# Kernel optimization log

Measured on AMD Instinct MI355X. Metric: run time of the kernel, lower is better.

Reference implementation:

```python
import jax, jax.numpy as jnp
import numpy as np

B, F, H, T = 32, 128, 256, 2048


def setup_inputs() -> dict:
    key = jax.random.key(0)
    ks = jax.random.split(key, 20)
    s = 0.05
    x = jax.random.normal(ks[0], (B, 1, T, F), dtype=jnp.float32)
    mask = (jax.random.uniform(ks[1], (B, 1, T, F)) < 0.5).astype(jnp.float32)
    delta = jax.random.uniform(ks[2], (B, 1, T, F), dtype=jnp.float32)  # time since last obs
    inp = jnp.concatenate([x, mask, delta], axis=1)  # [B, 3, T, F]
    p = lambda k, shape: jax.random.normal(k, shape, dtype=jnp.float32) * s
    return {
        "input": inp,
        "x_mean": p(ks[3], (F,)),
        # layer 0: input decay (diagonal), hidden decay, gates
        "w_dx": p(ks[4], (F,)), "b_dx": p(ks[5], (F,)),
        "W_dh0": p(ks[6], (F, H)), "b_dh0": p(ks[7], (H,)),
        "W0": p(ks[8], (F, 3 * H)), "U0": p(ks[9], (H, 3 * H)),
        "V0": p(ks[10], (F, 3 * H)), "b0": p(ks[11], (3 * H,)),
        # layer 1: hidden decay from delta, gates (input = prev layer hidden)
        "W_dh1": p(ks[12], (F, H)), "b_dh1": p(ks[13], (H,)),
        "W1": p(ks[14], (H, 3 * H)), "U1": p(ks[15], (H, 3 * H)),
        "V1": p(ks[16], (F, 3 * H)), "b1": p(ks[17], (3 * H,)),
    }


def _grud_cell(x_in, m, delta, h, W_dh, b_dh, W, U, V, b):
    # hidden-state decay from delta-time
    gamma_h = jnp.exp(-jax.nn.relu(delta @ W_dh + b_dh))  # [B,H]
    h = gamma_h * h
    pre = x_in @ W + m @ V + b                             # [B,3H]
    hU = h @ U[:, : 2 * H]                                 # r,z recurrent terms
    r = jax.nn.sigmoid(pre[:, :H] + hU[:, :H])
    z = jax.nn.sigmoid(pre[:, H : 2 * H] + hU[:, H : 2 * H])
    h_tilde = jnp.tanh(pre[:, 2 * H :] + (r * h) @ U[:, 2 * H :])
    return (1.0 - z) * h + z * h_tilde


def reference(input, x_mean, w_dx, b_dx, W_dh0, b_dh0, W0, U0, V0, b0,
              W_dh1, b_dh1, W1, U1, V1, b1):
    xs = jnp.moveaxis(input, 2, 0)  # [T, B, 3, F]
    x_last0 = jnp.broadcast_to(x_mean, (B, F))
    h0 = jnp.zeros((B, H), dtype=input.dtype)
    h1 = jnp.zeros((B, H), dtype=input.dtype)

    def step(carry, inp_t):
        x_last, h0, h1 = carry
        x, m, delta = inp_t[:, 0], inp_t[:, 1], inp_t[:, 2]  # [B,F] each
        # input decay toward empirical mean (GRU-D imputation)
        gamma_x = jnp.exp(-jax.nn.relu(delta * w_dx + b_dx))
        x_hat = m * x + (1.0 - m) * (gamma_x * x_last + (1.0 - gamma_x) * x_mean)
        h0n = _grud_cell(x_hat, m, delta, h0, W_dh0, b_dh0, W0, U0, V0, b0)
        h1n = _grud_cell(h0n, m, delta, h1, W_dh1, b_dh1, W1, U1, V1, b1)
        x_last_new = jnp.where(m > 0, x, x_last)  # update AFTER the cells, as in torch
        return (x_last_new, h0n, h1n), h1n

    _, ys = jax.lax.scan(step, (x_last0, h0, h1), xs)
    return ys  # [T, B, H]
```

## Files before the change

kernel.cpp:

```cpp
#include <hip/hip_runtime.h>

typedef _Float16 f16;
typedef _Float16 f16x2 __attribute__((ext_vector_type(2)));
typedef unsigned int u32;

#define CB 32
#define CF 128
#define CH 256
#define CT 2048
#define TCC 128
#define SEG 16
#define SLEN 128
#define SHBYTES 16896

static __device__ __forceinline__ f16x2 bc(u32 u){ return __builtin_bit_cast(f16x2, u); }
static __device__ __forceinline__ u32 packh2(float lo, float hi){ f16x2 v; v.x=(f16)lo; v.y=(f16)hi; return __builtin_bit_cast(u32, v); }

static __device__ __forceinline__ float dot2f(f16x2 a, f16x2 b, float c){
#if defined(__has_builtin)
#if __has_builtin(__builtin_amdgcn_fdot2)
  return __builtin_amdgcn_fdot2(a, b, c, false);
#else
  return c + (float)a.x*(float)b.x + (float)a.y*(float)b.y;
#endif
#else
  return c + (float)a.x*(float)b.x + (float)a.y*(float)b.y;
#endif
}
static __device__ __forceinline__ float dot4q(float acc, uint4 w, uint4 h){
  acc = dot2f(bc(w.x), bc(h.x), acc);
  acc = dot2f(bc(w.y), bc(h.y), acc);
  acc = dot2f(bc(w.z), bc(h.z), acc);
  acc = dot2f(bc(w.w), bc(h.w), acc);
  return acc;
}

#define PIN4(V) asm volatile("" : "+v"((V).x), "+v"((V).y), "+v"((V).z), "+v"((V).w))

#define RBAR() do { \
  asm volatile("s_waitcnt lgkmcnt(0)" ::: "memory"); \
  __builtin_amdgcn_s_barrier(); \
  asm volatile("" ::: "memory"); \
} while (0)

__global__ void init_hst(float* hst){
  int i = blockIdx.x*256 + threadIdx.x;
  if (i < 2*CB*CH) hst[i] = 0.f;
}

static __device__ __forceinline__ float wc0src(int k, int n, const float* W0, const float* V0, const float* Wdh0){
  if (k < 128) return (n < 768) ? W0[k*768 + n] : 0.f;
  if (k < 256) return (n < 768) ? V0[(k-128)*768 + n] : 0.f;
  return (n >= 768) ? Wdh0[(k-256)*256 + (n-768)] : 0.f;
}
static __device__ __forceinline__ float wc1src(int k, int n, const float* W1, const float* V1, const float* Wdh1){
  if (k < 256) return (n < 768) ? W1[k*768 + n] : 0.f;
  if (k < 384) return (n < 768) ? V1[(k-256)*768 + n] : 0.f;
  return (n >= 768) ? Wdh1[(k-384)*256 + (n-768)] : 0.f;
}
static __device__ __forceinline__ u32 wrz_pair(int flat, int jj, int L, const float* U){
  int p = L >> 2, q = L & 3;
  int cc = flat >> 3, j = flat & 7;
  int col = 4*p + cc;
  int pr = 32*q + 4*j + jj;
  return packh2(U[(2*pr)*768 + col], U[(2*pr+1)*768 + col]);
}
static __device__ __forceinline__ u32 wcc_pair(int flat, int jj, int L, const float* U){
  int p = L >> 2, q = L & 3;
  int cc2 = flat >> 3, j = flat & 7;
  int col = 512 + 2*p + cc2;
  int pr = 32*q + 4*j + jj;
  return packh2(U[(2*pr)*768 + col], U[(2*pr+1)*768 + col]);
}

__global__ __launch_bounds__(256) void pack_w(
    const float* __restrict__ W0, const float* __restrict__ V0, const float* __restrict__ Wdh0,
    const float* __restrict__ W1, const float* __restrict__ V1, const float* __restrict__ Wdh1,
    const float* __restrict__ U0, const float* __restrict__ U1,
    const float* __restrict__ b0, const float* __restrict__ bdh0,
    const float* __restrict__ b1, const float* __restrict__ bdh1,
    u32* __restrict__ WC0p, u32* __restrict__ WC1p,
    u32* __restrict__ WRZa, u32* __restrict__ WRZb,
    u32* __restrict__ WCCa, u32* __restrict__ WCCb,
    float* __restrict__ bias0, float* __restrict__ bias1){
  int idx = blockIdx.x*256 + threadIdx.x;
  if (idx < 196608){
    int k2 = idx >> 10, n = idx & 1023;
    WC0p[idx] = packh2(wc0src(2*k2, n, W0,V0,Wdh0), wc0src(2*k2+1, n, W0,V0,Wdh0));
  } else if (idx < 458752){
    int j = idx - 196608; int k2 = j >> 10, n = j & 1023;
    WC1p[j] = packh2(wc1src(2*k2, n, W1,V1,Wdh1), wc1src(2*k2+1, n, W1,V1,Wdh1));
  } else if (idx < 524288){
    int j = idx - 458752; int flat = j >> 11, L = (j >> 2) & 511, jj = j & 3;
    WRZa[j] = wrz_pair(flat, jj, L, U0);
  } else if (idx < 589824){
    int j = idx - 524288; int flat = j >> 11, L = (j >> 2) & 511, jj = j & 3;
    WRZb[j] = wrz_pair(flat, jj, L, U1);
  } else if (idx < 622592){
    int j = idx - 589824; int flat = j >> 11, L = (j >> 2) & 511, jj = j & 3;
    WCCa[j] = wcc_pair(flat, jj, L, U0);
  } else if (idx < 655360){
    int j = idx - 622592; int flat = j >> 11, L = (j >> 2) & 511, jj = j & 3;
    WCCb[j] = wcc_pair(flat, jj, L, U1);
  } else if (idx < 657408){
    int i = idx - 655360;
    if (i < 1024) bias0[i] = (i < 768) ? b0[i] : bdh0[i - 768];
    else { int j = i - 1024; bias1[j] = (j < 768) ? b1[j] : bdh1[j - 768]; }
  }
}

__global__ __launch_bounds__(256) void k1a(const float* __restrict__ in,
    float* __restrict__ segval, int* __restrict__ seghas){
  int tid = blockIdx.x*256 + threadIdx.x;
  int s = tid >> 12, chain = tid & 4095;
  int b = chain >> 7, f = chain & 127;
  const float* px = in + ((size_t)b*3 + 0)*CT*CF + f;
  const float* pm = in + ((size_t)b*3 + 1)*CT*CF + f;
  float last = 0.f; int has = 0;
  #pragma unroll 4
  for (int u = 0; u < SLEN; ++u){
    int t = s*SLEN + u;
    float m = pm[(size_t)t*CF], x = px[(size_t)t*CF];
    if (m > 0.f){ last = x; has = 1; }
  }
  segval[s*4096 + chain] = last;
  seghas[s*4096 + chain] = has;
}
__global__ __launch_bounds__(256) void k1b(const float* __restrict__ x_mean,
    const float* __restrict__ segval, const int* __restrict__ seghas, float* __restrict__ seed){
  int chain = blockIdx.x*256 + threadIdx.x;
  int f = chain & 127;
  float cur = x_mean[f];
  #pragma unroll
  for (int s = 0; s < SEG; ++s){
    seed[s*4096 + chain] = cur;
    if (seghas[s*4096 + chain]) cur = segval[s*4096 + chain];
  }
}
__global__ __launch_bounds__(256) void k1c(const float* __restrict__ in, const float* __restrict__ x_mean,
    const float* __restrict__ w_dx, const float* __restrict__ b_dx,
    const float* __restrict__ seed, f16* __restrict__ A){
  int tid = blockIdx.x*256 + threadIdx.x;
  int s = tid >> 12, chain = tid & 4095;
  int b = chain >> 7, f = chain & 127;
  const float wd = w_dx[f], bd = b_dx[f], xm = x_mean[f];
  const float* px = in + ((size_t)b*3 + 0)*CT*CF + f;
  const float* pm = in + ((size_t)b*3 + 1)*CT*CF + f;
  const float* pd = in + ((size_t)b*3 + 2)*CT*CF + f;
  float xl = seed[s*4096 + chain];
  #pragma unroll 4
  for (int u = 0; u < SLEN; ++u){
    int t = s*SLEN + u;
    float x = px[(size_t)t*CF], m = pm[(size_t)t*CF], d = pd[(size_t)t*CF];
    float gx = __expf(-fmaxf(d*wd + bd, 0.f));
    float xh = m*x + (1.f-m)*(gx*xl + (1.f-gx)*xm);
    f16* wq = A + ((size_t)t*CB + b)*384 + f;
    wq[0] = (f16)xh; wq[128] = (f16)m; wq[256] = (f16)d;
    xl = (m > 0.f) ? x : xl;
  }
}

static __device__ void gemm_tile(
    const u32* __restrict__ Aa, int lda, const u32* __restrict__ Ab, int ldb, int kasplit,
    int ktiles, const u32* __restrict__ Wp, const float* __restrict__ bias, float* __restrict__ Out,
    int row0, int n0, int tid, char* sm){
  u32 (*AsT)[68] = (u32 (*)[68])sm;
  u32 (*Bs)[64]  = (u32 (*)[64])(sm + 4352);
  const int tx = tid & 15, ty = tid >> 4;
  const int am = tid >> 2, akq = (tid & 3) * 4;
  const int bk = tid >> 4, bnq = (tid & 15) * 4;
  float acc[4][4] = {};
  for (int kt = 0; kt < ktiles; ++kt){
    int k2g = kt*16 + akq;
    uint4 ga;
    if (k2g < kasplit) ga = *(const uint4*)&Aa[(size_t)(row0 + am)*lda + k2g];
    else               ga = *(const uint4*)&Ab[(size_t)(row0 + am)*ldb + (k2g - kasplit)];
    uint4 gb = *(const uint4*)&Wp[(size_t)(kt*16 + bk)*1024 + n0 + bnq];
    __syncthreads();
    AsT[akq+0][am] = ga.x; AsT[akq+1][am] = ga.y; AsT[akq+2][am] = ga.z; AsT[akq+3][am] = ga.w;
    *(uint4*)&Bs[bk][bnq] = gb;
    __syncthreads();
    #pragma unroll
    for (int kk = 0; kk < 16; ++kk){
      uint4 bq = *(const uint4*)&Bs[kk][tx*4];
      uint4 aq = *(const uint4*)&AsT[kk][ty*4];
      f16x2 bv0 = bc(bq.x), bv1 = bc(bq.y), bv2 = bc(bq.z), bv3 = bc(bq.w);
      f16x2 av0 = bc(aq.x), av1 = bc(aq.y), av2 = bc(aq.z), av3 = bc(aq.w);
      acc[0][0] = dot2f(av0, bv0, acc[0][0]); acc[0][1] = dot2f(av0, bv1, acc[0][1]);
      acc[0][2] = dot2f(av0, bv2, acc[0][2]); acc[0][3] = dot2f(av0, bv3, acc[0][3]);
      acc[1][0] = dot2f(av1, bv0, acc[1][0]); acc[1][1] = dot2f(av1, bv1, acc[1][1]);
      acc[1][2] = dot2f(av1, bv2, acc[1][2]); acc[1][3] = dot2f(av1, bv3, acc[1][3]);
      acc[2][0] = dot2f(av2, bv0, acc[2][0]); acc[2][1] = dot2f(av2, bv1, acc[2][1]);
      acc[2][2] = dot2f(av2, bv2, acc[2][2]); acc[2][3] = dot2f(av2, bv3, acc[2][3]);
      acc[3][0] = dot2f(av3, bv0, acc[3][0]); acc[3][1] = dot2f(av3, bv1, acc[3][1]);
      acc[3][2] = dot2f(av3, bv2, acc[3][2]); acc[3][3] = dot2f(av3, bv3, acc[3][3]);
    }
  }
  const bool isg = (n0 >= 768);
  #pragma unroll
  for (int i = 0; i < 4; ++i){
    int r = row0 + ty*4 + i;
    int n = n0 + tx*4;
    float4 v;
    float* vv = (float*)&v;
    #pragma unroll
    for (int j = 0; j < 4; ++j){
      float x = acc[i][j] + bias[n + j];
      if (isg) x = __expf(-fmaxf(x, 0.f));
      vv[j] = x;
    }
    *(float4*)&Out[(size_t)r*1024 + n] = v;
  }
}

__global__ __launch_bounds__(512, 2) void mega(
    const float* __restrict__ O0r, const float* __restrict__ O1r,
    const u32* __restrict__ WRZa, const u32* __restrict__ WRZb,
    const u32* __restrict__ WCCa, const u32* __restrict__ WCCb,
    float* __restrict__ hst, f16* __restrict__ h0cw, float* __restrict__ out,
    int t0_l1, int n0, int n1, int g0n, int g1n,
    const u32* __restrict__ g0a, float* __restrict__ g0out,
    const u32* __restrict__ g1a, const u32* __restrict__ g1b, float* __restrict__ g1out,
    const u32* __restrict__ WC0p, const u32* __restrict__ WC1p,
    const float* __restrict__ bias0, const float* __restrict__ bias1){
  extern __shared__ __align__(16) char smraw[];
  const int L = threadIdx.x;
  if (blockIdx.x >= 64){
    int gb = blockIdx.x - 64;
    int st = L >> 8, t2 = L & 255;
    char* smst = smraw + st*8448;
    if (gb < g0n){
      int tile = gb*2 + st;
      gemm_tile(g0a, 192, g0a, 192, 192, 12, WC0p, bias0, g0out, (tile>>4)*64, (tile&15)*64, t2, smst);
    } else {
      int tile = (gb - g0n)*2 + st;
      gemm_tile(g1a, 128, g1b, 192, 128, 16, WC1p, bias1, g1out, (tile>>4)*64, (tile&15)*64, t2, smst);
    }
    return;
  }
  const int role = blockIdx.x >> 5;
  const int b = blockIdx.x & 31;
  const int steps = role ? n1 : n0;
  if (steps == 0) return;
  const float* O = role ? O1r : O0r;
  const u32* WRZ = role ? WRZb : WRZa;
  const u32* WCC = role ? WCCb : WCCa;
  float* hcarry = hst + role*CB*CH;

  f16*  hdh_  = (f16*)(smraw);
  f16*  rh_   = (f16*)(smraw + 640);
  float* hdf  = (float*)(smraw + 1280);
  float* zz   = (float*)(smraw + 2304);

  uint4 wrz[32];
  #pragma unroll
  for (int i = 0; i < 32; ++i) wrz[i] = *(const uint4*)&WRZ[((size_t)i*512 + L)*4];
  uint4 wcc[16];
  #pragma unroll
  for (int i = 0; i < 16; ++i) wcc[i] = *(const uint4*)&WCC[((size_t)i*512 + L)*4];
  #pragma unroll
  for (int i = 0; i < 32; ++i) PIN4(wrz[i]);
  #pragma unroll
  for (int i = 0; i < 16; ++i) PIN4(wcc[i]);

  const int p = L >> 2, q = L & 3;
  size_t row = (size_t)b*1024;
  if (L < 256){
    float hd = O[row + 768 + L] * hcarry[b*256 + L];
    hdf[L] = hd; hdh_[(L>>6)*80 + (L&63)] = (f16)hd;
  }
  float prz = O[row + L];
  const int e2 = 2*p + (q & 1);
  float pc = (q < 2) ? O[row + 512 + e2] : 0.f;
  const char* hqb = (const char*)hdh_ + q*160;
  const char* rqb = (const char*)rh_ + q*160;
  __syncthreads();

  for (int lt = 0; lt < steps; ++lt){
    size_t nrow = row + (size_t)CB*1024;
    float nprz = 0.f, npc = 0.f, ngex = 0.f;
    if (lt + 1 < steps){
      nprz = O[nrow + L];
      if (q < 2){ npc = O[nrow + 512 + e2]; ngex = O[nrow + 768 + e2]; }
    }
    float hdL = (L < 256) ? hdf[L] : 0.f;
    float hd2 = hdf[e2];
    float a0=0.f, a1=0.f, a2=0.f, a3=0.f;
    #pragma unroll
    for (int j = 0; j < 8; ++j){
      uint4 h = ((const uint4*)hqb)[j];
      a0 = dot4q(a0, wrz[j],      h);
      a1 = dot4q(a1, wrz[8 + j],  h);
      a2 = dot4q(a2, wrz[16 + j], h);
      a3 = dot4q(a3, wrz[24 + j], h);
    }
    a0 += __shfl_xor(a0, 1); a1 += __shfl_xor(a1, 1); a2 += __shfl_xor(a2, 1); a3 += __shfl_xor(a3, 1);
    a0 += __shfl_xor(a0, 2); a1 += __shfl_xor(a1, 2); a2 += __shfl_xor(a2, 2); a3 += __shfl_xor(a3, 2);
    float sum1 = (q == 0) ? a0 : (q == 1) ? a1 : (q == 2) ? a2 : a3;
    float s1 = 1.f/(1.f + __expf(-(sum1 + prz)));
    if (L < 256) rh_[(L>>6)*80 + (L&63)] = (f16)(s1 * hdL);
    else zz[L - 256] = s1;
    RBAR();
    float z = zz[e2];
    float b0_=0.f, b1_=0.f;
    #pragma unroll
    for (int j = 0; j < 8; ++j){
      uint4 r = ((const uint4*)rqb)[j];
      b0_ = dot4q(b0_, wcc[j],     r);
      b1_ = dot4q(b1_, wcc[8 + j], r);
    }
    b0_ += __shfl_xor(b0_, 1); b1_ += __shfl_xor(b1_, 1);
    b0_ += __shfl_xor(b0_, 2); b1_ += __shfl_xor(b1_, 2);
    if (q < 2){
      float sumc = (q & 1) ? b1_ : b0_;
      float v = pc + sumc;
      float e = __expf(2.f*v);
      float ct = 1.f - 2.f/(1.f + e);
      float hd = hd2;
      float hn = hd + z*(ct - hd);
      float hdn = ngex*hn;
      hdf[e2] = hdn; hdh_[(e2>>6)*80 + (e2&63)] = (f16)hdn;
      if (role == 0) h0cw[((size_t)lt*CB + b)*256 + e2] = (f16)hn;
      else           out[((size_t)(t0_l1 + lt)*CB + b)*256 + e2] = hn;
      if (lt == steps-1) hcarry[b*256 + e2] = hn;
    }
    prz = nprz; pc = npc;
    row = nrow;
    RBAR();
  }
}

extern "C" void kernel_launch(void* const* d_in, const int* in_sizes, int n_in,
                              void* d_out, int out_size, void* d_ws, size_t ws_size,
                              hipStream_t stream){
  const float* input  = (const float*)d_in[0];
  const float* x_mean = (const float*)d_in[1];
  const float* w_dx   = (const float*)d_in[2];
  const float* b_dx   = (const float*)d_in[3];
  const float* Wdh0   = (const float*)d_in[4];
  const float* bdh0   = (const float*)d_in[5];
  const float* W0     = (const float*)d_in[6];
  const float* U0     = (const float*)d_in[7];
  const float* V0     = (const float*)d_in[8];
  const float* b0     = (const float*)d_in[9];
  const float* Wdh1   = (const float*)d_in[10];
  const float* bdh1   = (const float*)d_in[11];
  const float* W1     = (const float*)d_in[12];
  const float* U1     = (const float*)d_in[13];
  const float* V1     = (const float*)d_in[14];
  const float* b1     = (const float*)d_in[15];
  float* out = (float*)d_out;

  hipFuncSetAttribute((const void*)mega, hipFuncAttributeMaxDynamicSharedMemorySize, SHBYTES);

  char* base = (char*)d_ws;
  size_t off = 0;
  auto take = [&](size_t bytes)->char*{
    char* p = base + off;
    off = (off + bytes + 255) & ~(size_t)255;
    return p;
  };
  f16*  IN0h  = (f16*) take((size_t)CT*CB*384*2);
  u32*  WC0p  = (u32*) take((size_t)192*1024*4);
  u32*  WC1p  = (u32*) take((size_t)256*1024*4);
  u32*  WRZa  = (u32*) take((size_t)32*512*4*4);
  u32*  WRZb  = (u32*) take((size_t)32*512*4*4);
  u32*  WCCa  = (u32*) take((size_t)16*512*4*4);
  u32*  WCCb  = (u32*) take((size_t)16*512*4*4);
  float* bias0= (float*)take(1024*4);
  float* bias1= (float*)take(1024*4);
  float* hst  = (float*)take((size_t)2*CB*CH*4);
  float* segv = (float*)take((size_t)SEG*4096*4);
  int*   segh = (int*)  take((size_t)SEG*4096*4);
  float* seed = (float*)take((size_t)SEG*4096*4);
  float* O0b[2], *O1b[2]; f16* h0b[2];
  O0b[0] = (float*)take((size_t)TCC*CB*1024*4);
  O0b[1] = (float*)take((size_t)TCC*CB*1024*4);
  O1b[0] = (float*)take((size_t)TCC*CB*1024*4);
  O1b[1] = (float*)take((size_t)TCC*CB*1024*4);
  h0b[0] = (f16*)  take((size_t)TCC*CB*CH*2);
  h0b[1] = (f16*)  take((size_t)TCC*CB*CH*2);

  hipLaunchKernelGGL(init_hst, dim3(64), dim3(256), 0, stream, hst);
  hipLaunchKernelGGL(pack_w, dim3((657408 + 255)/256), dim3(256), 0, stream,
      W0, V0, Wdh0, W1, V1, Wdh1, U0, U1, b0, bdh0, b1, bdh1,
      WC0p, WC1p, WRZa, WRZb, WCCa, WCCb, bias0, bias1);
  hipLaunchKernelGGL(k1a, dim3(256), dim3(256), 0, stream, input, segv, segh);
  hipLaunchKernelGGL(k1b, dim3(16), dim3(256), 0, stream, x_mean, segv, segh, seed);
  hipLaunchKernelGGL(k1c, dim3(256), dim3(256), 0, stream, input, x_mean, w_dx, b_dx, seed, IN0h);

  const u32* IN0p = (const u32*)IN0h;
  const int nch = CT / TCC;
  for (int i = -1; i <= nch + 1; ++i){
    int r0 = (i >= 0 && i < nch) ? 1 : 0;
    int r1 = (i >= 2 && i < nch + 2) ? 1 : 0;
    int g0 = (i + 1 >= 0 && i + 1 < nch) ? 1 : 0;
    int g1 = (i - 1 >= 0 && i - 1 < nch) ? 1 : 0;
    int g0n = g0 ? 512 : 0, g1n = g1 ? 512 : 0;
    const float* O0r = O0b[i & 1];
    const float* O1r = O1b[i & 1];
    f16* h0cw = h0b[i & 1];
    const u32* g0a = IN0p + (size_t)(i+1)*TCC*CB*192;
    float* g0out = O0b[(i+1) & 1];
    const u32* g1a = (const u32*)h0b[(i-1) & 1];
    const u32* g1b = IN0p + (size_t)(i-1)*TCC*CB*192 + 64;
    float* g1out = O1b[(i-1) & 1];
    hipLaunchKernelGGL(mega, dim3(64 + g0n + g1n), dim3(512), SHBYTES, stream,
        O0r, O1r, WRZa, WRZb, WCCa, WCCb, hst, h0cw, out,
        (i-2)*TCC, r0 ? TCC : 0, r1 ? TCC : 0, g0n, g1n,
        g0a, g0out, g1a, g1b, g1out,
        WC0p, WC1p, bias0, bias1);
  }
}
```

Baseline: 3.760 ms.

## Batch recurrent GRU steps over 16 rows per block using MFMA

The recurrent part of each GRU-D cell now runs in 4 blocks, each handling 16 batch rows and both gate matmuls with 16x16x32 f16 MFMA instructions, instead of 64 blocks each doing one batch row with fdot2 dot products and cross-lane shuffles. The U weights are repacked into MFMA fragment layout and hidden states are staged in padded LDS tiles. This cuts per-step instruction count and shuffle reductions, but it leaves far fewer blocks on the serial critical path and uses more LDS per block.

```diff
diff --git a/kernel.cpp b/kernel.cpp
--- a/kernel.cpp
+++ b/kernel.cpp
@@ -2,6 +2,8 @@
 
 typedef _Float16 f16;
 typedef _Float16 f16x2 __attribute__((ext_vector_type(2)));
+typedef _Float16 f16x8 __attribute__((ext_vector_type(8)));
+typedef float f32x4 __attribute__((ext_vector_type(4)));
 typedef unsigned int u32;
 
 #define CB 32
@@ -11,9 +13,10 @@
 #define TCC 128
 #define SEG 16
 #define SLEN 128
-#define SHBYTES 16896
+#define SHBYTES 58368
 
 static __device__ __forceinline__ f16x2 bc(u32 u){ return __builtin_bit_cast(f16x2, u); }
+static __device__ __forceinline__ f16x8 bch8(uint4 u){ return __builtin_bit_cast(f16x8, u); }
 static __device__ __forceinline__ u32 packh2(float lo, float hi){ f16x2 v; v.x=(f16)lo; v.y=(f16)hi; return __builtin_bit_cast(u32, v); }
 
 static __device__ __forceinline__ float dot2f(f16x2 a, f16x2 b, float c){
@@ -27,13 +30,6 @@
   return c + (float)a.x*(float)b.x + (float)a.y*(float)b.y;
 #endif
 }
-static __device__ __forceinline__ float dot4q(float acc, uint4 w, uint4 h){
-  acc = dot2f(bc(w.x), bc(h.x), acc);
-  acc = dot2f(bc(w.y), bc(h.y), acc);
-  acc = dot2f(bc(w.z), bc(h.z), acc);
-  acc = dot2f(bc(w.w), bc(h.w), acc);
-  return acc;
-}
 
 #define PIN4(V) asm volatile("" : "+v"((V).x), "+v"((V).y), "+v"((V).z), "+v"((V).w))
 
@@ -58,19 +54,19 @@
   if (k < 384) return (n < 768) ? V1[(k-256)*768 + n] : 0.f;
   return (n >= 768) ? Wdh1[(k-384)*256 + (n-768)] : 0.f;
 }
-static __device__ __forceinline__ u32 wrz_pair(int flat, int jj, int L, const float* U){
-  int p = L >> 2, q = L & 3;
-  int cc = flat >> 3, j = flat & 7;
-  int col = 4*p + cc;
-  int pr = 32*q + 4*j + jj;
-  return packh2(U[(2*pr)*768 + col], U[(2*pr+1)*768 + col]);
-}
-static __device__ __forceinline__ u32 wcc_pair(int flat, int jj, int L, const float* U){
-  int p = L >> 2, q = L & 3;
-  int cc2 = flat >> 3, j = flat & 7;
-  int col = 512 + 2*p + cc2;
-  int pr = 32*q + 4*j + jj;
-  return packh2(U[(2*pr)*768 + col], U[(2*pr+1)*768 + col]);
+static __device__ __forceinline__ u32 wfrz_src(int j, const float* U){
+  int fi = j >> 11, Lt = (j >> 2) & 511, d = j & 3;
+  int wv = Lt >> 6, lg = (Lt >> 4) & 3, li = Lt & 15;
+  int col = 64*wv + 16*(fi >> 3) + li;
+  int k0 = (fi & 7)*32 + lg*8 + 2*d;
+  return packh2(U[k0*768 + col], U[(k0+1)*768 + col]);
+}
+static __device__ __forceinline__ u32 wfc_src(int j, const float* U){
+  int fi = j >> 11, Lt = (j >> 2) & 511, d = j & 3;
+  int wv = Lt >> 6, lg = (Lt >> 4) & 3, li = Lt & 15;
+  int col = 512 + 32*wv + 16*(fi >> 3) + li;
+  int k0 = (fi & 7)*32 + lg*8 + 2*d;
+  return packh2(U[k0*768 + col], U[(k0+1)*768 + col]);
 }
 
 __global__ __launch_bounds__(256) void pack_w(
@@ -80,8 +76,8 @@
     const float* __restrict__ b0, const float* __restrict__ bdh0,
     const float* __restrict__ b1, const float* __restrict__ bdh1,
     u32* __restrict__ WC0p, u32* __restrict__ WC1p,
-    u32* __restrict__ WRZa, u32* __restrict__ WRZb,
-    u32* __restrict__ WCCa, u32* __restrict__ WCCb,
+    u32* __restrict__ WF0rz, u32* __restrict__ WF1rz,
+    u32* __restrict__ WF0c, u32* __restrict__ WF1c,
     float* __restrict__ bias0, float* __restrict__ bias1){
   int idx = blockIdx.x*256 + threadIdx.x;
   if (idx < 196608){
@@ -91,17 +87,13 @@
     int j = idx - 196608; int k2 = j >> 10, n = j & 1023;
     WC1p[j] = packh2(wc1src(2*k2, n, W1,V1,Wdh1), wc1src(2*k2+1, n, W1,V1,Wdh1));
   } else if (idx < 524288){
-    int j = idx - 458752; int flat = j >> 11, L = (j >> 2) & 511, jj = j & 3;
-    WRZa[j] = wrz_pair(flat, jj, L, U0);
+    WF0rz[idx - 458752] = wfrz_src(idx - 458752, U0);
   } else if (idx < 589824){
-    int j = idx - 524288; int flat = j >> 11, L = (j >> 2) & 511, jj = j & 3;
-    WRZb[j] = wrz_pair(flat, jj, L, U1);
+    WF1rz[idx - 524288] = wfrz_src(idx - 524288, U1);
   } else if (idx < 622592){
-    int j = idx - 589824; int flat = j >> 11, L = (j >> 2) & 511, jj = j & 3;
-    WCCa[j] = wcc_pair(flat, jj, L, U0);
+    WF0c[idx - 589824] = wfc_src(idx - 589824, U0);
   } else if (idx < 655360){
-    int j = idx - 622592; int flat = j >> 11, L = (j >> 2) & 511, jj = j & 3;
-    WCCb[j] = wcc_pair(flat, jj, L, U1);
+    WF1c[idx - 622592] = wfc_src(idx - 622592, U1);
   } else if (idx < 657408){
     int i = idx - 655360;
     if (i < 1024) bias0[i] = (i < 768) ? b0[i] : bdh0[i - 768];
@@ -215,8 +207,8 @@
 
 __global__ __launch_bounds__(512, 2) void mega(
     const float* __restrict__ O0r, const float* __restrict__ O1r,
-    const u32* __restrict__ WRZa, const u32* __restrict__ WRZb,
-    const u32* __restrict__ WCCa, const u32* __restrict__ WCCb,
+    const u32* __restrict__ WF0rz, const u32* __restrict__ WF1rz,
+    const u32* __restrict__ WF0c, const u32* __restrict__ WF1c,
     float* __restrict__ hst, f16* __restrict__ h0cw, float* __restrict__ out,
     int t0_l1, int n0, int n1, int g0n, int g1n,
     const u32* __restrict__ g0a, float* __restrict__ g0out,
@@ -225,8 +217,8 @@
     const float* __restrict__ bias0, const float* __restrict__ bias1){
   extern __shared__ __align__(16) char smraw[];
   const int L = threadIdx.x;
-  if (blockIdx.x >= 64){
-    int gb = blockIdx.x - 64;
+  if (blockIdx.x >= 4){
+    int gb = blockIdx.x - 4;
     int st = L >> 8, t2 = L & 255;
     char* smst = smraw + st*8448;
     if (gb < g0n){
@@ -238,94 +230,141 @@
     }
     return;
   }
-  const int role = blockIdx.x >> 5;
-  const int b = blockIdx.x & 31;
+  const int role = blockIdx.x >> 1;
+  const int half = blockIdx.x & 1;
   const int steps = role ? n1 : n0;
   if (steps == 0) return;
   const float* O = role ? O1r : O0r;
-  const u32* WRZ = role ? WRZb : WRZa;
-  const u32* WCC = role ? WCCb : WCCa;
-  float* hcarry = hst + role*CB*CH;
-
-  f16*  hdh_  = (f16*)(smraw);
-  f16*  rh_   = (f16*)(smraw + 640);
-  float* hdf  = (float*)(smraw + 1280);
-  float* zz   = (float*)(smraw + 2304);
+  const u32* WFrz = role ? WF1rz : WF0rz;
+  const u32* WFc  = role ? WF1c  : WF0c;
+  const int r0g = half*16;
+  float* hcarry = hst + role*CB*CH + r0g*CH;
+
+  f16*  h16  = (f16*)smraw;
+  f16*  rh16 = (f16*)(smraw + 8704);
+  float* hdF = (float*)(smraw + 17408);
+  float* zF  = (float*)(smraw + 37888);
+
+  const int l  = L & 63, wv = L >> 6;
+  const int lg = l >> 4, li = l & 15;
 
   uint4 wrz[32];
   #pragma unroll
-  for (int i = 0; i < 32; ++i) wrz[i] = *(const uint4*)&WRZ[((size_t)i*512 + L)*4];
-  uint4 wcc[16];
-  #pragma unroll
-  for (int i = 0; i < 16; ++i) wcc[i] = *(const uint4*)&WCC[((size_t)i*512 + L)*4];
+  for (int i = 0; i < 32; ++i) wrz[i] = *(const uint4*)&WFrz[((size_t)i*512 + L)*4];
+  uint4 wcf[16];
+  #pragma unroll
+  for (int i = 0; i < 16; ++i) wcf[i] = *(const uint4*)&WFc[((size_t)i*512 + L)*4];
   #pragma unroll
   for (int i = 0; i < 32; ++i) PIN4(wrz[i]);
   #pragma unroll
-  for (int i = 0; i < 16; ++i) PIN4(wcc[i]);
-
-  const int p = L >> 2, q = L & 3;
-  size_t row = (size_t)b*1024;
-  if (L < 256){
-    float hd = O[row + 768 + L] * hcarry[b*256 + L];
-    hdf[L] = hd; hdh_[(L>>6)*80 + (L&63)] = (f16)hd;
-  }
-  float prz = O[row + L];
-  const int e2 = 2*p + (q & 1);
-  float pc = (q < 2) ? O[row + 512 + e2] : 0.f;
-  const char* hqb = (const char*)hdh_ + q*160;
-  const char* rqb = (const char*)rh_ + q*160;
+  for (int i = 0; i < 16; ++i) PIN4(wcf[i]);
+
+  __builtin_amdgcn_s_setprio(1);
+
+  {
+    int base = L*8;
+    int row = base >> 8, j0 = base & 255;
+    const float* gp = O + ((size_t)(r0g + row))*1024 + 768 + j0;
+    float hd[8];
+    #pragma unroll
+    for (int e = 0; e < 8; ++e){
+      hd[e] = gp[e] * hcarry[row*256 + j0 + e];
+      hdF[(j0+e)*20 + row] = hd[e];
+    }
+    uint4 hw;
+    hw.x = packh2(hd[0], hd[1]); hw.y = packh2(hd[2], hd[3]);
+    hw.z = packh2(hd[4], hd[5]); hw.w = packh2(hd[6], hd[7]);
+    *(uint4*)((char*)h16 + row*544 + j0*2) = hw;
+  }
+  float pre1[16];
+  #pragma unroll
+  for (int nt = 0; nt < 4; ++nt)
+    #pragma unroll
+    for (int i = 0; i < 4; ++i)
+      pre1[nt*4+i] = O[((size_t)(r0g + 4*lg + i))*1024 + 64*wv + 16*nt + li];
   __syncthreads();
 
   for (int lt = 0; lt < steps; ++lt){
-    size_t nrow = row + (size_t)CB*1024;
-    float nprz = 0.f, npc = 0.f, ngex = 0.f;
-    if (lt + 1 < steps){
-      nprz = O[nrow + L];
-      if (q < 2){ npc = O[nrow + 512 + e2]; ngex = O[nrow + 768 + e2]; }
-    }
-    float hdL = (L < 256) ? hdf[L] : 0.f;
-    float hd2 = hdf[e2];
-    float a0=0.f, a1=0.f, a2=0.f, a3=0.f;
-    #pragma unroll
-    for (int j = 0; j < 8; ++j){
-      uint4 h = ((const uint4*)hqb)[j];
-      a0 = dot4q(a0, wrz[j],      h);
-      a1 = dot4q(a1, wrz[8 + j],  h);
-      a2 = dot4q(a2, wrz[16 + j], h);
-      a3 = dot4q(a3, wrz[24 + j], h);
-    }
-    a0 += __shfl_xor(a0, 1); a1 += __shfl_xor(a1, 1); a2 += __shfl_xor(a2, 1); a3 += __shfl_xor(a3, 1);
-    a0 += __shfl_xor(a0, 2); a1 += __shfl_xor(a1, 2); a2 += __shfl_xor(a2, 2); a3 += __shfl_xor(a3, 2);
-    float sum1 = (q == 0) ? a0 : (q == 1) ? a1 : (q == 2) ? a2 : a3;
-    float s1 = 1.f/(1.f + __expf(-(sum1 + prz)));
-    if (L < 256) rh_[(L>>6)*80 + (L&63)] = (f16)(s1 * hdL);
-    else zz[L - 256] = s1;
+    const size_t rb = (size_t)(lt*32 + r0g);
+    f32x4 acc0 = {0.f,0.f,0.f,0.f}, acc1 = acc0, acc2 = acc0, acc3 = acc0;
+    #pragma unroll
+    for (int kt = 0; kt < 8; ++kt){
+      f16x8 a = bch8(*(const uint4*)((const char*)h16 + li*544 + kt*64 + lg*16));
+      acc0 = __builtin_amdgcn_mfma_f32_16x16x32_f16(a, bch8(wrz[kt]),      acc0, 0,0,0);
+      acc1 = __builtin_amdgcn_mfma_f32_16x16x32_f16(a, bch8(wrz[8 + kt]),  acc1, 0,0,0);
+      acc2 = __builtin_amdgcn_mfma_f32_16x16x32_f16(a, bch8(wrz[16 + kt]), acc2, 0,0,0);
+      acc3 = __builtin_amdgcn_mfma_f32_16x16x32_f16(a, bch8(wrz[24 + kt]), acc3, 0,0,0);
+    }
+    if (wv < 4){
+      #pragma unroll
+      for (int nt = 0; nt < 4; ++nt){
+        f32x4 ac = (nt==0)?acc0:(nt==1)?acc1:(nt==2)?acc2:acc3;
+        int j1 = 64*wv + 16*nt + li;
+        f32x4 hd4 = *(const f32x4*)&hdF[j1*20 + lg*4];
+        #pragma unroll
+        for (int i = 0; i < 4; ++i){
+          float s1 = 1.f/(1.f + __expf(-(ac[i] + pre1[nt*4+i])));
+          rh16[(4*lg+i)*272 + j1] = (f16)(s1 * hd4[i]);
+        }
+      }
+    } else {
+      #pragma unroll
+      for (int nt = 0; nt < 4; ++nt){
+        f32x4 ac = (nt==0)?acc0:(nt==1)?acc1:(nt==2)?acc2:acc3;
+        int jz = 64*(wv-4) + 16*nt + li;
+        f32x4 zv;
+        #pragma unroll
+        for (int i = 0; i < 4; ++i) zv[i] = 1.f/(1.f + __expf(-(ac[i] + pre1[nt*4+i])));
+        *(f32x4*)&zF[jz*20 + lg*4] = zv;
+      }
+    }
     RBAR();
-    float z = zz[e2];
-    float b0_=0.f, b1_=0.f;
-    #pragma unroll
-    for (int j = 0; j < 8; ++j){
-      uint4 r = ((const uint4*)rqb)[j];
-      b0_ = dot4q(b0_, wcc[j],     r);
-      b1_ = dot4q(b1_, wcc[8 + j], r);
-    }
-    b0_ += __shfl_xor(b0_, 1); b1_ += __shfl_xor(b1_, 1);
-    b0_ += __shfl_xor(b0_, 2); b1_ += __shfl_xor(b1_, 2);
-    if (q < 2){
-      float sumc = (q & 1) ? b1_ : b0_;
-      float v = pc + sumc;
-      float e = __expf(2.f*v);
-      float ct = 1.f - 2.f/(1.f + e);
-      float hd = hd2;
-      float hn = hd + z*(ct - hd);
-      float hdn = ngex*hn;
-      hdf[e2] = hdn; hdh_[(e2>>6)*80 + (e2&63)] = (f16)hdn;
-      if (role == 0) h0cw[((size_t)lt*CB + b)*256 + e2] = (f16)hn;
-      else           out[((size_t)(t0_l1 + lt)*CB + b)*256 + e2] = hn;
-      if (lt == steps-1) hcarry[b*256 + e2] = hn;
-    }
-    prz = nprz; pc = npc;
-    row = nrow;
+    const int ltn = (lt+1 < steps) ? lt+1 : lt;
+    float pc[8], gmn[8];
+    #pragma unroll
+    for (int nt = 0; nt < 2; ++nt)
+      #pragma unroll
+      for (int i = 0; i < 4; ++i){
+        int j2 = 32*wv + 16*nt + li;
+        pc[nt*4+i]  = O[(rb + 4*lg + i)*1024 + 512 + j2];
+        gmn[nt*4+i] = O[((size_t)(ltn*32 + r0g) + 4*lg + i)*1024 + 768 + j2];
+      }
+    f32x4 acc4 = {0.f,0.f,0.f,0.f}, acc5 = acc4;
+    #pragma unroll
+    for (int kt = 0; kt < 8; ++kt){
+      f16x8 a = bch8(*(const uint4*)((const char*)rh16 + li*544 + kt*64 + lg*16));
+      acc4 = __builtin_amdgcn_mfma_f32_16x16x32_f16(a, bch8(wcf[kt]),     acc4, 0,0,0);
+      acc5 = __builtin_amdgcn_mfma_f32_16x16x32_f16(a, bch8(wcf[8 + kt]), acc5, 0,0,0);
+    }
+    #pragma unroll
+    for (int nt = 0; nt < 2; ++nt){
+      f32x4 ac = (nt==0)?acc4:acc5;
+      int j2 = 32*wv + 16*nt + li;
+      f32x4 zv  = *(const f32x4*)&zF[j2*20 + lg*4];
+      f32x4 hd4 = *(const f32x4*)&hdF[j2*20 + lg*4];
+      f32x4 hdn4;
+      #pragma unroll
+      for (int i = 0; i < 4; ++i){
+        float v = ac[i] + pc[nt*4+i];
+        float e = __expf(2.f*v);
+        float ct = 1.f - 2.f/(1.f + e);
+        float hn = hd4[i] + zv[i]*(ct - hd4[i]);
+        if (role == 0) h0cw[(rb + 4*lg + i)*256 + j2] = (f16)hn;
+        else           out[((size_t)((t0_l1 + lt)*32 + r0g) + 4*lg + i)*256 + j2] = hn;
+        if (lt == steps-1) hcarry[(4*lg+i)*256 + j2] = hn;
+        float hdn = gmn[nt*4+i]*hn;
+        hdn4[i] = hdn;
+        h16[(4*lg+i)*272 + j2] = (f16)hdn;
+      }
+      *(f32x4*)&hdF[j2*20 + lg*4] = hdn4;
+    }
+    if (lt+1 < steps){
+      #pragma unroll
+      for (int nt = 0; nt < 4; ++nt)
+        #pragma unroll
+        for (int i = 0; i < 4; ++i)
+          pre1[nt*4+i] = O[((size_t)((lt+1)*32 + r0g) + 4*lg + i)*1024 + 64*wv + 16*nt + li];
+    }
     RBAR();
   }
 }
@@ -363,10 +402,10 @@
   f16*  IN0h  = (f16*) take((size_t)CT*CB*384*2);
   u32*  WC0p  = (u32*) take((size_t)192*1024*4);
   u32*  WC1p  = (u32*) take((size_t)256*1024*4);
-  u32*  WRZa  = (u32*) take((size_t)32*512*4*4);
-  u32*  WRZb  = (u32*) take((size_t)32*512*4*4);
-  u32*  WCCa  = (u32*) take((size_t)16*512*4*4);
-  u32*  WCCb  = (u32*) take((size_t)16*512*4*4);
+  u32*  WF0rz = (u32*) take((size_t)32*512*4*4);
+  u32*  WF1rz = (u32*) take((size_t)32*512*4*4);
+  u32*  WF0c  = (u32*) take((size_t)16*512*4*4);
+  u32*  WF1c  = (u32*) take((size_t)16*512*4*4);
   float* bias0= (float*)take(1024*4);
   float* bias1= (float*)take(1024*4);
   float* hst  = (float*)take((size_t)2*CB*CH*4);
@@ -384,7 +423,7 @@
   hipLaunchKernelGGL(init_hst, dim3(64), dim3(256), 0, stream, hst);
   hipLaunchKernelGGL(pack_w, dim3((657408 + 255)/256), dim3(256), 0, stream,
       W0, V0, Wdh0, W1, V1, Wdh1, U0, U1, b0, bdh0, b1, bdh1,
-      WC0p, WC1p, WRZa, WRZb, WCCa, WCCb, bias0, bias1);
+      WC0p, WC1p, WF0rz, WF1rz, WF0c, WF1c, bias0, bias1);
   hipLaunchKernelGGL(k1a, dim3(256), dim3(256), 0, stream, input, segv, segh);
   hipLaunchKernelGGL(k1b, dim3(16), dim3(256), 0, stream, x_mean, segv, segh, seed);
   hipLaunchKernelGGL(k1c, dim3(256), dim3(256), 0, stream, input, x_mean, w_dx, b_dx, seed, IN0h);
@@ -405,8 +444,8 @@
     const u32* g1a = (const u32*)h0b[(i-1) & 1];
     const u32* g1b = IN0p + (size_t)(i-1)*TCC*CB*192 + 64;
     float* g1out = O1b[(i-1) & 1];
-    hipLaunchKernelGGL(mega, dim3(64 + g0n + g1n), dim3(512), SHBYTES, stream,
-        O0r, O1r, WRZa, WRZb, WCCa, WCCb, hst, h0cw, out,
+    hipLaunchKernelGGL(mega, dim3(4 + g0n + g1n), dim3(512), SHBYTES, stream,
+        O0r, O1r, WF0rz, WF1rz, WF0c, WF1c, hst, h0cw, out,
         (i-2)*TCC, r0 ? TCC : 0, r1 ? TCC : 0, g0n, g1n,
         g0a, g0out, g1a, g1b, g1out,
         WC0p, WC1p, bias0, bias1);
```

Result: slower. 10.04 ms (+167.0%).
